# Optimization experiments

Hardware: AMD Instinct MI355X
Metric: run time of the kernel (lower is better)

Reference implementation:

```python
import jax, jax.numpy as jnp
import numpy as np

N_NODES = 100000
N_EDGES = 1600000
UNITS = 256
N_LAYERS = 4          # model_layers
NUM_GRAPHS = 512
IN_FEAT = 9


def _glorot(key, shape):
    lim = float(np.sqrt(6.0 / (shape[0] + shape[1])))
    return jax.random.uniform(key, shape, jnp.float32, -lim, lim)


def setup_inputs() -> dict:
    key = jax.random.key(0)
    ks = jax.random.split(key, 16)
    x = jax.random.normal(ks[0], (N_NODES, IN_FEAT), jnp.float32)
    edge_index = jax.random.randint(ks[1], (2, N_EDGES), 0, N_NODES, jnp.int64)
    batch = jnp.sort(jax.random.randint(ks[2], (N_NODES,), 0, NUM_GRAPHS, jnp.int64))
    Win = _glorot(ks[3], (IN_FEAT, UNITS))
    bin_ = jnp.zeros((UNITS,), jnp.float32)
    Ws = jnp.stack([_glorot(ks[4 + i], (UNITS, UNITS)) for i in range(N_LAYERS - 1)])
    bs = jnp.zeros((N_LAYERS - 1, UNITS), jnp.float32)
    fc1_w = _glorot(ks[8], (UNITS, UNITS))
    fc1_b = jnp.zeros((UNITS,), jnp.float32)
    fc2_w = _glorot(ks[9], (UNITS, 32))
    fc2_b = jnp.zeros((32,), jnp.float32)
    fc3_w = _glorot(ks[10], (32, 1))
    fc3_b = jnp.zeros((1,), jnp.float32)
    return dict(x=x, edge_index=edge_index, batch=batch, Win=Win, bin_=bin_,
                Ws=Ws, bs=bs, fc1_w=fc1_w, fc1_b=fc1_b, fc2_w=fc2_w,
                fc2_b=fc2_b, fc3_w=fc3_w, fc3_b=fc3_b)


def _gcn_conv(x, W, b, src, dst, dinv):
    # PyG GCNConv: h = xW ; out = D^-1/2 (A+I) D^-1/2 h + b  (self-loops added)
    h = x @ W                                     # [N, d]
    norm = dinv[src] * dinv[dst]                  # [E]
    agg = jnp.zeros_like(h).at[dst].add(h[src] * norm[:, None])
    agg = agg + h * (dinv * dinv)[:, None]        # self-loop term
    return agg + b


def reference(x, edge_index, batch, Win, bin_, Ws, bs,
              fc1_w, fc1_b, fc2_w, fc2_b, fc3_w, fc3_b):
    src, dst = edge_index[0], edge_index[1]
    # degree with self-loops
    deg = jnp.zeros((N_NODES,), jnp.float32).at[dst].add(1.0) + 1.0
    dinv = jax.lax.rsqrt(deg)

    h = jnp.tanh(_gcn_conv(x, Win, bin_, src, dst, dinv))
    for i in range(N_LAYERS - 1):
        h = jnp.tanh(_gcn_conv(h, Ws[i], bs[i], src, dst, dinv))
        # dropout: identity at inference
    h = jnp.tanh(h @ fc1_w + fc1_b)
    h = jnp.tanh(h @ fc2_w + fc2_b)
    h = h @ fc3_w + fc3_b                          # [N, 1]
    # global mean pool over graphs
    sums = jax.ops.segment_sum(h, batch, num_segments=NUM_GRAPHS)      # [G, 1]
    cnts = jax.ops.segment_sum(jnp.ones((N_NODES,), jnp.float32), batch,
                               num_segments=NUM_GRAPHS)
    pooled = sums / jnp.maximum(cnts, 1.0)[:, None]
    return jax.nn.sigmoid(pooled)
```

## Files before the change

kernel.cpp:

```cpp
#include <hip/hip_runtime.h>
#include <math.h>

#define N_NODES 100000
#define N_EDGES 1600000
#define UNITS   256
#define NGRAPH  512
#define IN_FEAT 9
#define NB_SCAN ((N_NODES + 255) / 256)
#define NBUK    ((N_NODES + 255) / 256)
#define BCAP    8192
#define EPB     16384
#define NPB     ((N_EDGES + EPB - 1) / EPB)

typedef short bf16x8 __attribute__((ext_vector_type(8)));
typedef float f32x4  __attribute__((ext_vector_type(4)));
typedef float f32x2  __attribute__((ext_vector_type(2)));

__device__ __forceinline__ float bflo(unsigned int u) {
  return __builtin_bit_cast(float, u << 16);
}
__device__ __forceinline__ float bfhi(unsigned int u) {
  return __builtin_bit_cast(float, u & 0xffff0000u);
}
__device__ __forceinline__ unsigned short f2bf(float f) {
  unsigned int u = __builtin_bit_cast(unsigned int, f);
  u += 0x7fffu + ((u >> 16) & 1u);
  return (unsigned short)(u >> 16);
}

__device__ __forceinline__ int swz(int row, int byteInRow) {
  return row * 128 + (byteInRow ^ ((row & 7) << 4));
}


__global__ __launch_bounds__(256) void k_part(const int* __restrict__ ei,
                                              int* __restrict__ bcnt,
                                              uint2* __restrict__ bstore) {
  __shared__ int hist[NBUK];
  __shared__ int base[NBUK];
  int tid = threadIdx.x;
  int e0 = blockIdx.x * EPB;
  for (int i = tid; i < NBUK; i += 256) hist[i] = 0;
  __syncthreads();
  #pragma unroll 4
  for (int j = 0; j < EPB / 256; ++j) {
    int e = e0 + j * 256 + tid;
    if (e < N_EDGES) atomicAdd(&hist[ei[N_EDGES + e] >> 8], 1);
  }
  __syncthreads();
  for (int i = tid; i < NBUK; i += 256) {
    int h = hist[i];
    base[i] = h ? atomicAdd(&bcnt[i], h) : 0;
    hist[i] = 0;
  }
  __syncthreads();
  #pragma unroll 4
  for (int j = 0; j < EPB / 256; ++j) {
    int e = e0 + j * 256 + tid;
    if (e < N_EDGES) {
      int s = ei[e];
      int d = ei[N_EDGES + e];
      int b = d >> 8;
      int pos = base[b] + atomicAdd(&hist[b], 1);
      bstore[(size_t)b * BCAP + pos] = make_uint2((unsigned)s, (unsigned)d);
    }
  }
}

__global__ __launch_bounds__(256) void k_cnt(const int* __restrict__ bcnt,
                                             const uint2* __restrict__ bstore,
                                             int* __restrict__ cnt) {
  __shared__ int h[256];
  int b = blockIdx.x, tid = threadIdx.x;
  h[tid] = 0;
  __syncthreads();
  int nE = bcnt[b];
  for (int i = tid; i < nE; i += 256)
    atomicAdd(&h[bstore[(size_t)b * BCAP + i].y & 255], 1);
  __syncthreads();
  int node = b * 256 + tid;
  if (node < N_NODES) cnt[node] = h[tid];
}

__global__ __launch_bounds__(256) void k_colfill(const int* __restrict__ bcnt,
                                                 const uint2* __restrict__ bstore,
                                                 const int* __restrict__ row_ptr,
                                                 int* __restrict__ col) {
  __shared__ int cur[256];
  int b = blockIdx.x, tid = threadIdx.x;
  int node = b * 256 + tid;
  cur[tid] = (node < N_NODES) ? row_ptr[node] : 0;
  __syncthreads();
  int nE = bcnt[b];
  for (int i = tid; i < nE; i += 256) {
    uint2 sd = bstore[(size_t)b * BCAP + i];
    int pos = atomicAdd(&cur[sd.y & 255], 1);
    col[pos] = (int)sd.x;
  }
}

__global__ __launch_bounds__(256) void k_bsum(const int* __restrict__ cnt,
                                              int* __restrict__ bsum) {
  __shared__ int wsS[4];
  int b = blockIdx.x, tid = threadIdx.x, lane = tid & 63, w = tid >> 6;
  int idx = b * 256 + tid;
  int s = (idx < N_NODES) ? cnt[idx] : 0;
  #pragma unroll
  for (int m = 32; m >= 1; m >>= 1) s += __shfl_xor(s, m);
  if (lane == 0) wsS[w] = s;
  __syncthreads();
  if (tid == 0) bsum[b] = wsS[0] + wsS[1] + wsS[2] + wsS[3];
}

__global__ __launch_bounds__(512) void k_bscan(int* __restrict__ bsum) {
  __shared__ int wsS[8];
  int tid = threadIdx.x, lane = tid & 63, w = tid >> 6;
  int v = (tid < NB_SCAN) ? bsum[tid] : 0;
  int s = v;
  #pragma unroll
  for (int off = 1; off < 64; off <<= 1) {
    int t = __shfl_up(s, off);
    if (lane >= off) s += t;
  }
  if (lane == 63) wsS[w] = s;
  __syncthreads();
  int woff = 0;
  #pragma unroll
  for (int i = 0; i < 8; ++i) woff += (i < w) ? wsS[i] : 0;
  if (tid < NB_SCAN) bsum[tid] = woff + s - v;
}

__global__ __launch_bounds__(256) void k_scan3(const int* __restrict__ cnt,
                                               const int* __restrict__ bsum,
                                               int* __restrict__ row_ptr) {
  __shared__ int wsS[4];
  int b = blockIdx.x, tid = threadIdx.x, lane = tid & 63, w = tid >> 6;
  int idx = b * 256 + tid;
  int v = (idx < N_NODES) ? cnt[idx] : 0;
  int s = v;
  #pragma unroll
  for (int off = 1; off < 64; off <<= 1) {
    int t = __shfl_up(s, off);
    if (lane >= off) s += t;
  }
  if (lane == 63) wsS[w] = s;
  __syncthreads();
  int woff = 0;
  #pragma unroll
  for (int i = 0; i < 4; ++i) woff += (i < w) ? wsS[i] : 0;
  if (idx < N_NODES) row_ptr[idx] = bsum[b] + woff + s - v;
  if (idx == 0) row_ptr[N_NODES] = N_EDGES;
}

__global__ void k_dinv(const int* __restrict__ cnt, float* __restrict__ dinv) {
  int n = blockIdx.x * blockDim.x + threadIdx.x;
  if (n < N_NODES) dinv[n] = rsqrtf((float)cnt[n] + 1.0f);
}

__global__ void k_bounds(const int* __restrict__ batch, int* __restrict__ starts) {
  int g = blockIdx.x * blockDim.x + threadIdx.x;
  if (g > NGRAPH) return;
  if (g == NGRAPH) { starts[g] = N_NODES; return; }
  int lo = 0, hi = N_NODES;
  while (lo < hi) { int m = (lo + hi) >> 1; if (batch[m] < g) lo = m + 1; else hi = m; }
  starts[g] = lo;
}


__global__ void k_cvtW(const float* __restrict__ Ws, const float* __restrict__ fc1_w,
                       unsigned short* __restrict__ Wt) {
  int idx = blockIdx.x * 256 + threadIdx.x;
  int m = idx >> 16;
  int r = idx & 65535;
  int n = r >> 8;
  int k = r & 255;
  const float* src = (m < 3) ? (Ws + (size_t)m * 65536) : fc1_w;
  Wt[idx] = f2bf(src[k * 256 + n]);
}

__global__ void k_cvtW2(const float* __restrict__ fc2_w, unsigned short* __restrict__ Wt2) {
  int idx = blockIdx.x * 256 + threadIdx.x;
  int n = idx >> 8;
  int k = idx & 255;
  Wt2[idx] = f2bf(fc2_w[k * 32 + n]);
}

__global__ void k_scalex(const float* __restrict__ x, const float* __restrict__ dinv,
                         float* __restrict__ xs) {
  int idx = blockIdx.x * blockDim.x + threadIdx.x;
  if (idx < N_NODES * IN_FEAT) xs[idx] = x[idx] * dinv[idx / IN_FEAT];
}


__global__ void k_agg9(const float* __restrict__ xs, const int* __restrict__ row_ptr,
                       const int* __restrict__ col, const float* __restrict__ dinv,
                       float* __restrict__ p0) {
  int n = blockIdx.x * blockDim.x + threadIdx.x;
  if (n >= N_NODES) return;
  float acc[IN_FEAT];
  #pragma unroll
  for (int j = 0; j < IN_FEAT; ++j) acc[j] = xs[n * IN_FEAT + j];
  int beg = row_ptr[n], end = row_ptr[n + 1];
  for (int e = beg; e < end; ++e) {
    int s = col[e];
    #pragma unroll
    for (int j = 0; j < IN_FEAT; ++j) acc[j] += xs[s * IN_FEAT + j];
  }
  float dn = dinv[n];
  #pragma unroll
  for (int j = 0; j < IN_FEAT; ++j) p0[n * IN_FEAT + j] = dn * acc[j];
}

__global__ __launch_bounds__(256) void k_agg256(
    const unsigned int* __restrict__ hs8,
    const int* __restrict__ row_ptr, const int* __restrict__ col,
    const float* __restrict__ dinv, unsigned short* __restrict__ p) {
  int wid = threadIdx.x >> 6;
  int lane = threadIdx.x & 63;
  int n = blockIdx.x * 4 + wid;
  if (n >= N_NODES) return;
  unsigned int q = hs8[(size_t)n * 64 + lane];
  f32x2 lo = __builtin_amdgcn_cvt_pk_f32_fp8(q, false);
  f32x2 hi = __builtin_amdgcn_cvt_pk_f32_fp8(q, true);
  float a0 = lo[0], a1 = lo[1], a2 = hi[0], a3 = hi[1];
  int e = row_ptr[n], end = row_ptr[n + 1];
  for (; e + 8 <= end; e += 8) {
    int s[8];
    unsigned int qq[8];
    #pragma unroll
    for (int j = 0; j < 8; ++j) s[j] = col[e + j];
    #pragma unroll
    for (int j = 0; j < 8; ++j) qq[j] = hs8[(size_t)s[j] * 64 + lane];
    #pragma unroll
    for (int j = 0; j < 8; ++j) {
      f32x2 l2 = __builtin_amdgcn_cvt_pk_f32_fp8(qq[j], false);
      f32x2 h2 = __builtin_amdgcn_cvt_pk_f32_fp8(qq[j], true);
      a0 += l2[0]; a1 += l2[1]; a2 += h2[0]; a3 += h2[1];
    }
  }
  if (e + 4 <= end) {
    int s[4];
    unsigned int qq[4];
    #pragma unroll
    for (int j = 0; j < 4; ++j) s[j] = col[e + j];
    #pragma unroll
    for (int j = 0; j < 4; ++j) qq[j] = hs8[(size_t)s[j] * 64 + lane];
    #pragma unroll
    for (int j = 0; j < 4; ++j) {
      f32x2 l2 = __builtin_amdgcn_cvt_pk_f32_fp8(qq[j], false);
      f32x2 h2 = __builtin_amdgcn_cvt_pk_f32_fp8(qq[j], true);
      a0 += l2[0]; a1 += l2[1]; a2 += h2[0]; a3 += h2[1];
    }
    e += 4;
  }
  for (; e < end; ++e) {
    unsigned int q0 = hs8[(size_t)col[e] * 64 + lane];
    f32x2 l2 = __builtin_amdgcn_cvt_pk_f32_fp8(q0, false);
    f32x2 h2 = __builtin_amdgcn_cvt_pk_f32_fp8(q0, true);
    a0 += l2[0]; a1 += l2[1]; a2 += h2[0]; a3 += h2[1];
  }
  float dn = dinv[n];
  uint2 o;
  o.x = (unsigned int)f2bf(dn * a0) | ((unsigned int)f2bf(dn * a1) << 16);
  o.y = (unsigned int)f2bf(dn * a2) | ((unsigned int)f2bf(dn * a3) << 16);
  *(uint2*)(p + (size_t)n * UNITS + lane * 4) = o;
}


__global__ __launch_bounds__(256) void k_gemm9(const float* __restrict__ p0,
                                               const float* __restrict__ Win,
                                               const float* __restrict__ bin,
                                               const float* __restrict__ scale,
                                               unsigned char* __restrict__ h8) {
  __shared__ float pS[32][IN_FEAT];
  int tid = threadIdx.x;
  int row0 = blockIdx.x * 32;
  for (int i = tid; i < 32 * IN_FEAT; i += 256) {
    int r = i / IN_FEAT;
    pS[r][i % IN_FEAT] = (row0 + r < N_NODES) ? p0[(size_t)row0 * IN_FEAT + i] : 0.0f;
  }
  float wcol[IN_FEAT];
  #pragma unroll
  for (int k = 0; k < IN_FEAT; ++k) wcol[k] = Win[k * UNITS + tid];
  float b = bin[tid];
  __syncthreads();
  for (int r = 0; r < 32; ++r) {
    int gr = row0 + r;
    if (gr >= N_NODES) break;
    float a = b;
    #pragma unroll
    for (int k = 0; k < IN_FEAT; ++k) a += pS[r][k] * wcol[k];
    float v = scale[gr] * tanhf(a);
    float vn = __shfl_xor(v, 1);
    if ((tid & 1) == 0) {
      unsigned int pk = __builtin_amdgcn_cvt_pk_fp8_f32(v, vn, 0, false);
      *(unsigned short*)(h8 + (size_t)gr * UNITS + tid) = (unsigned short)pk;
    }
  }
}

__global__ __launch_bounds__(256, 4) void k_gemm_bf16(
    const unsigned short* __restrict__ A,
    const unsigned short* __restrict__ Wt,
    const float* __restrict__ bias,
    const float* __restrict__ scale,
    void* __restrict__ Cout, int out_fp8,
    int M) {
  __shared__ __align__(16) char lds[33792];
  char* Bs = lds;
  unsigned short (*Cs)[264] = (unsigned short(*)[264])lds;

  const int tid = threadIdx.x;
  const int w = tid >> 6;
  const int l = tid & 63;
  const int l15 = l & 15;
  const int blk = l >> 4;
  const int wr = w >> 1, wc = w & 1;
  const int row0 = blockIdx.x * 64;

  const int sr = tid >> 3;
  const int sc = (tid & 7) * 16;

  const unsigned short* aRow[2];
  #pragma unroll
  for (int rf = 0; rf < 2; ++rf) {
    int gr = row0 + 32 * wr + rf * 16 + l15;
    if (gr >= M) gr = M - 1;
    aRow[rf] = A + (size_t)gr * UNITS + 8 * blk;
  }

  f32x4 acc[2][8];
  #pragma unroll
  for (int rf = 0; rf < 2; ++rf)
    #pragma unroll
    for (int cf = 0; cf < 8; ++cf) acc[rf][cf] = (f32x4){0.f, 0.f, 0.f, 0.f};

  for (int ks = 0; ks < 4; ++ks) {
    const int k0 = ks * 64;
    if (ks) __syncthreads();
    #pragma unroll
    for (int i = 0; i < 8; ++i) {
      int n = sr + i * 32;
      uint4 v = *(const uint4*)(Wt + (size_t)n * UNITS + k0 + (sc >> 1));
      *(uint4*)(Bs + swz(n, sc)) = v;
    }
    __syncthreads();
    #pragma unroll
    for (int kc = 0; kc < 2; ++kc) {
      bf16x8 a[2];
      #pragma unroll
      for (int rf = 0; rf < 2; ++rf)
        a[rf] = *(const bf16x8*)(aRow[rf] + k0 + kc * 32);
      #pragma unroll
      for (int cf = 0; cf < 8; ++cf) {
        bf16x8 b = *(const bf16x8*)(Bs + swz(128 * wc + cf * 16 + l15, kc * 64 + blk * 16));
        acc[0][cf] = __builtin_amdgcn_mfma_f32_16x16x32_bf16(a[0], b, acc[0][cf], 0, 0, 0);
        acc[1][cf] = __builtin_amdgcn_mfma_f32_16x16x32_bf16(a[1], b, acc[1][cf], 0, 0, 0);
      }
    }
  }

  __syncthreads();
  float dvv[2][4];
  #pragma unroll
  for (int rf = 0; rf < 2; ++rf)
    #pragma unroll
    for (int reg = 0; reg < 4; ++reg) {
      int gr = row0 + 32 * wr + rf * 16 + 4 * blk + reg;
      dvv[rf][reg] = scale ? scale[gr < M ? gr : M - 1] : 1.0f;
    }
  #pragma unroll
  for (int cf = 0; cf < 8; ++cf) {
    float bcol = bias[128 * wc + cf * 16 + l15];
    #pragma unroll
    for (int rf = 0; rf < 2; ++rf) {
      #pragma unroll
      for (int reg = 0; reg < 4; ++reg) {
        float v = dvv[rf][reg] * tanhf(acc[rf][cf][reg] + bcol);
        Cs[32 * wr + rf * 16 + 4 * blk + reg][128 * wc + cf * 16 + l15] = f2bf(v);
      }
    }
  }
  __syncthreads();
  if (out_fp8) {
    unsigned char* C8 = (unsigned char*)Cout;
    #pragma unroll
    for (int j = 0; j < 8; ++j) {
      int flat = tid + j * 256;
      int r = flat >> 5;
      int c = flat & 31;
      int gr = row0 + r;
      if (gr < M) {
        uint4 v = *(const uint4*)&Cs[r][c * 8];
        uint2 u;
        u.x = __builtin_amdgcn_cvt_pk_fp8_f32(bflo(v.x), bfhi(v.x), 0, false);
        u.x = __builtin_amdgcn_cvt_pk_fp8_f32(bflo(v.y), bfhi(v.y), u.x, true);
        u.y = __builtin_amdgcn_cvt_pk_fp8_f32(bflo(v.z), bfhi(v.z), 0, false);
        u.y = __builtin_amdgcn_cvt_pk_fp8_f32(bflo(v.w), bfhi(v.w), u.y, true);
        *(uint2*)(C8 + (size_t)gr * UNITS + c * 8) = u;
      }
    }
  } else {
    unsigned short* C = (unsigned short*)Cout;
    #pragma unroll
    for (int j = 0; j < 8; ++j) {
      int flat = tid + j * 256;
      int r = flat >> 5;
      int c = flat & 31;
      int gr = row0 + r;
      if (gr < M) {
        uint4 v = *(const uint4*)&Cs[r][c * 8];
        *(uint4*)(C + (size_t)gr * UNITS + c * 8) = v;
      }
    }
  }
}


__global__ __launch_bounds__(256) void k_fc23(
    const unsigned short* __restrict__ H,
    const unsigned short* __restrict__ Wt2,
    const float* __restrict__ b2,
    const float* __restrict__ w3, const float* __restrict__ b3,
    float* __restrict__ ns, int M) {
  const int tid = threadIdx.x;
  const int w = tid >> 6;
  const int l = tid & 63;
  const int l15 = l & 15;
  const int blk = l >> 4;
  const int row0 = blockIdx.x * 64 + 16 * w;

  int r = row0 + l15;
  int rc = r < M ? r : M - 1;
  const unsigned short* aPtr = H + (size_t)rc * UNITS + 8 * blk;
  const unsigned short* bPtr = Wt2 + (size_t)l15 * UNITS + 8 * blk;

  f32x4 acc0 = (f32x4){0.f, 0.f, 0.f, 0.f};
  f32x4 acc1 = (f32x4){0.f, 0.f, 0.f, 0.f};
  #pragma unroll
  for (int k0 = 0; k0 < UNITS; k0 += 32) {
    bf16x8 a  = *(const bf16x8*)(aPtr + k0);
    bf16x8 b0 = *(const bf16x8*)(bPtr + k0);
    bf16x8 b1 = *(const bf16x8*)(bPtr + 16 * UNITS + k0);
    acc0 = __builtin_amdgcn_mfma_f32_16x16x32_bf16(a, b0, acc0, 0, 0, 0);
    acc1 = __builtin_amdgcn_mfma_f32_16x16x32_bf16(a, b1, acc1, 0, 0, 0);
  }

  float c0 = b2[l15], c1 = b2[16 + l15];
  float w30 = w3[l15], w31 = w3[16 + l15];
  float b3v = b3[0];
  #pragma unroll
  for (int reg = 0; reg < 4; ++reg) {
    float part = tanhf(acc0[reg] + c0) * w30 + tanhf(acc1[reg] + c1) * w31;
    #pragma unroll
    for (int m = 8; m >= 1; m >>= 1) part += __shfl_xor(part, m);
    int gr = row0 + 4 * blk + reg;
    if (l15 == 0 && gr < M) ns[gr] = part + b3v;
  }
}

__global__ __launch_bounds__(64) void k_pool(const float* __restrict__ ns,
                                             const int* __restrict__ starts,
                                             float* __restrict__ out) {
  int g = blockIdx.x;
  int lane = threadIdx.x;
  int s = starts[g], e = starts[g + 1];
  float acc = 0.0f;
  for (int i = s + lane; i < e; i += 64) acc += ns[i];
  #pragma unroll
  for (int m = 32; m >= 1; m >>= 1) acc += __shfl_xor(acc, m);
  if (lane == 0) {
    float mean = acc / fmaxf((float)(e - s), 1.0f);
    out[g] = 1.0f / (1.0f + expf(-mean));
  }
}


extern "C" void kernel_launch(void* const* d_in, const int* in_sizes, int n_in,
                              void* d_out, int out_size, void* d_ws, size_t ws_size,
                              hipStream_t stream) {
  const float* x     = (const float*)d_in[0];
  const int*   ei    = (const int*)d_in[1];
  const int*   batch = (const int*)d_in[2];
  const float* Win   = (const float*)d_in[3];
  const float* bin_  = (const float*)d_in[4];
  const float* Ws    = (const float*)d_in[5];
  const float* bs    = (const float*)d_in[6];
  const float* fc1_w = (const float*)d_in[7];
  const float* fc1_b = (const float*)d_in[8];
  const float* fc2_w = (const float*)d_in[9];
  const float* fc2_b = (const float*)d_in[10];
  const float* fc3_w = (const float*)d_in[11];
  const float* fc3_b = (const float*)d_in[12];
  float* out = (float*)d_out;

  char* ws = (char*)d_ws;
  size_t off = 0;
  auto alloc = [&](size_t bytes) {
    size_t o = off;
    off = (off + bytes + 255) & ~(size_t)255;
    return o;
  };
  int*   cnt     = (int*)(ws + alloc(N_NODES * 4));
  int*   row_ptr = (int*)(ws + alloc((N_NODES + 1) * 4));
  float* dinv    = (float*)(ws + alloc(N_NODES * 4));
  int*   col     = (int*)(ws + alloc((size_t)N_EDGES * 4));
  int*   bsum    = (int*)(ws + alloc(NB_SCAN * 4));
  int*   bcnt    = (int*)(ws + alloc(NBUK * 4));
  uint2* bstore  = (uint2*)(ws + alloc((size_t)NBUK * BCAP * 8));
  int*   starts  = (int*)(ws + alloc((NGRAPH + 1) * 4));
  float* ns      = (float*)(ws + alloc(N_NODES * 4));
  float* xs      = (float*)(ws + alloc((size_t)N_NODES * IN_FEAT * 4));
  float* p0      = (float*)(ws + alloc((size_t)N_NODES * IN_FEAT * 4));
  unsigned short* Wt   = (unsigned short*)(ws + alloc((size_t)4 * UNITS * UNITS * 2));
  unsigned short* Wt2  = (unsigned short*)(ws + alloc((size_t)32 * UNITS * 2));
  unsigned char*  h8a  = (unsigned char*)(ws + alloc((size_t)N_NODES * UNITS));
  unsigned char*  h8b  = (unsigned char*)(ws + alloc((size_t)N_NODES * UNITS));
  unsigned short* pbf  = (unsigned short*)(ws + alloc((size_t)N_NODES * UNITS * 2));
  unsigned short* hbf  = (unsigned short*)(ws + alloc((size_t)N_NODES * UNITS * 2));

  hipMemsetAsync(bcnt, 0, NBUK * 4, stream);

  k_cvtW<<<(4 * UNITS * UNITS) / 256, 256, 0, stream>>>(Ws, fc1_w, Wt);
  k_cvtW2<<<32, 256, 0, stream>>>(fc2_w, Wt2);

  k_part<<<NPB, 256, 0, stream>>>(ei, bcnt, bstore);
  k_cnt<<<NBUK, 256, 0, stream>>>(bcnt, bstore, cnt);
  k_bsum<<<NB_SCAN, 256, 0, stream>>>(cnt, bsum);
  k_bscan<<<1, 512, 0, stream>>>(bsum);
  k_scan3<<<NB_SCAN, 256, 0, stream>>>(cnt, bsum, row_ptr);
  k_dinv<<<(N_NODES + 255) / 256, 256, 0, stream>>>(cnt, dinv);
  k_colfill<<<NBUK, 256, 0, stream>>>(bcnt, bstore, row_ptr, col);
  k_bounds<<<3, 256, 0, stream>>>(batch, starts);

  k_scalex<<<(N_NODES * IN_FEAT + 255) / 256, 256, 0, stream>>>(x, dinv, xs);
  k_agg9<<<(N_NODES + 255) / 256, 256, 0, stream>>>(xs, row_ptr, col, dinv, p0);
  k_gemm9<<<(N_NODES + 31) / 32, 256, 0, stream>>>(p0, Win, bin_, dinv, h8a);

  int ggrid = (N_NODES + 63) / 64;
  k_agg256<<<(N_NODES + 3) / 4, 256, 0, stream>>>((const unsigned int*)h8a, row_ptr, col, dinv, pbf);
  k_gemm_bf16<<<ggrid, 256, 0, stream>>>(pbf, Wt + (size_t)0 * UNITS * UNITS,
                                         bs + (size_t)0 * UNITS, dinv, h8b, 1, N_NODES);
  k_agg256<<<(N_NODES + 3) / 4, 256, 0, stream>>>((const unsigned int*)h8b, row_ptr, col, dinv, pbf);
  k_gemm_bf16<<<ggrid, 256, 0, stream>>>(pbf, Wt + (size_t)1 * UNITS * UNITS,
                                         bs + (size_t)1 * UNITS, dinv, h8a, 1, N_NODES);
  k_agg256<<<(N_NODES + 3) / 4, 256, 0, stream>>>((const unsigned int*)h8a, row_ptr, col, dinv, pbf);
  k_gemm_bf16<<<ggrid, 256, 0, stream>>>(pbf, Wt + (size_t)2 * UNITS * UNITS,
                                         bs + (size_t)2 * UNITS, nullptr, hbf, 0, N_NODES);

  k_gemm_bf16<<<ggrid, 256, 0, stream>>>(hbf, Wt + (size_t)3 * UNITS * UNITS,
                                         fc1_b, nullptr, pbf, 0, N_NODES);

  k_fc23<<<(N_NODES + 63) / 64, 256, 0, stream>>>(pbf, Wt2, fc2_b, fc3_w, fc3_b, ns, N_NODES);

  k_pool<<<NGRAPH, 64, 0, stream>>>(ns, starts, out);
}
```

Measured before the change: 561.9 us.

## Fuse neighbor aggregation into GEMM kernel via LDS-staged A tile

Merges the per-layer sparse aggregation kernel with the following dense bf16 GEMM. Each block gathers 64 node rows into a swizzled LDS A tile and multiplies it directly with the weights, so the bf16 aggregated buffer is never written to or read back from global memory. The cost is 64KB of LDS per block with a 2-blocks occupancy bound, and the gather phase can no longer overlap with other blocks' MFMA work as freely. The plain GEMM kernel is reduced to the fc1 case.

Result: slower. 888.6 us (+58.1%).

```diff
diff --git a/kernel.cpp b/kernel.cpp
--- a/kernel.cpp
+++ b/kernel.cpp
@@ -31,6 +31,9 @@
 __device__ __forceinline__ int swz(int row, int byteInRow) {
   return row * 128 + (byteInRow ^ ((row & 7) << 4));
 }
+__device__ __forceinline__ int swzA(int row, int byteInRow) {
+  return row * 512 + (byteInRow ^ ((row & 7) << 4));
+}
 
 
 __global__ __launch_bounds__(256) void k_part(const int* __restrict__ ei,
@@ -210,62 +213,6 @@
   #pragma unroll
   for (int j = 0; j < IN_FEAT; ++j) p0[n * IN_FEAT + j] = dn * acc[j];
 }
-
-__global__ __launch_bounds__(256) void k_agg256(
-    const unsigned int* __restrict__ hs8,
-    const int* __restrict__ row_ptr, const int* __restrict__ col,
-    const float* __restrict__ dinv, unsigned short* __restrict__ p) {
-  int wid = threadIdx.x >> 6;
-  int lane = threadIdx.x & 63;
-  int n = blockIdx.x * 4 + wid;
-  if (n >= N_NODES) return;
-  unsigned int q = hs8[(size_t)n * 64 + lane];
-  f32x2 lo = __builtin_amdgcn_cvt_pk_f32_fp8(q, false);
-  f32x2 hi = __builtin_amdgcn_cvt_pk_f32_fp8(q, true);
-  float a0 = lo[0], a1 = lo[1], a2 = hi[0], a3 = hi[1];
-  int e = row_ptr[n], end = row_ptr[n + 1];
-  for (; e + 8 <= end; e += 8) {
-    int s[8];
-    unsigned int qq[8];
-    #pragma unroll
-    for (int j = 0; j < 8; ++j) s[j] = col[e + j];
-    #pragma unroll
-    for (int j = 0; j < 8; ++j) qq[j] = hs8[(size_t)s[j] * 64 + lane];
-    #pragma unroll
-    for (int j = 0; j < 8; ++j) {
-      f32x2 l2 = __builtin_amdgcn_cvt_pk_f32_fp8(qq[j], false);
-      f32x2 h2 = __builtin_amdgcn_cvt_pk_f32_fp8(qq[j], true);
-      a0 += l2[0]; a1 += l2[1]; a2 += h2[0]; a3 += h2[1];
-    }
-  }
-  if (e + 4 <= end) {
-    int s[4];
-    unsigned int qq[4];
-    #pragma unroll
-    for (int j = 0; j < 4; ++j) s[j] = col[e + j];
-    #pragma unroll
-    for (int j = 0; j < 4; ++j) qq[j] = hs8[(size_t)s[j] * 64 + lane];
-    #pragma unroll
-    for (int j = 0; j < 4; ++j) {
-      f32x2 l2 = __builtin_amdgcn_cvt_pk_f32_fp8(qq[j], false);
-      f32x2 h2 = __builtin_amdgcn_cvt_pk_f32_fp8(qq[j], true);
-      a0 += l2[0]; a1 += l2[1]; a2 += h2[0]; a3 += h2[1];
-    }
-    e += 4;
-  }
-  for (; e < end; ++e) {
-    unsigned int q0 = hs8[(size_t)col[e] * 64 + lane];
-    f32x2 l2 = __builtin_amdgcn_cvt_pk_f32_fp8(q0, false);
-    f32x2 h2 = __builtin_amdgcn_cvt_pk_f32_fp8(q0, true);
-    a0 += l2[0]; a1 += l2[1]; a2 += h2[0]; a3 += h2[1];
-  }
-  float dn = dinv[n];
-  uint2 o;
-  o.x = (unsigned int)f2bf(dn * a0) | ((unsigned int)f2bf(dn * a1) << 16);
-  o.y = (unsigned int)f2bf(dn * a2) | ((unsigned int)f2bf(dn * a3) << 16);
-  *(uint2*)(p + (size_t)n * UNITS + lane * 4) = o;
-}
-
 
 __global__ __launch_bounds__(256) void k_gemm9(const float* __restrict__ p0,
                                                const float* __restrict__ Win,
@@ -299,12 +246,182 @@
   }
 }
 
+
+__global__ __launch_bounds__(256, 2) void k_agg_gemm(
+    const unsigned int* __restrict__ hs8,
+    const int* __restrict__ row_ptr, const int* __restrict__ col,
+    const float* __restrict__ dinv,
+    const unsigned short* __restrict__ Wt,
+    const float* __restrict__ bias,
+    const float* __restrict__ scale,
+    void* __restrict__ Cout, int out_fp8, int M) {
+  __shared__ __align__(16) char lds[65536];
+  char* As = lds;
+  char* Bs = lds + 32768;
+  unsigned short* CsA = (unsigned short*)lds;
+
+  const int tid = threadIdx.x;
+  const int w = tid >> 6;
+  const int lane = tid & 63;
+  const int l15 = lane & 15;
+  const int blk = lane >> 4;
+  const int wr = w >> 1, wc = w & 1;
+  const int row0 = blockIdx.x * 64;
+
+  for (int rr = 0; rr < 16; ++rr) {
+    int r = w * 16 + rr;
+    int n = row0 + r;
+    float a0 = 0.f, a1 = 0.f, a2 = 0.f, a3 = 0.f;
+    if (n < M) {
+      unsigned int q = hs8[(size_t)n * 64 + lane];
+      f32x2 lo = __builtin_amdgcn_cvt_pk_f32_fp8(q, false);
+      f32x2 hi = __builtin_amdgcn_cvt_pk_f32_fp8(q, true);
+      a0 = lo[0]; a1 = lo[1]; a2 = hi[0]; a3 = hi[1];
+      int e = row_ptr[n], end = row_ptr[n + 1];
+      for (; e + 8 <= end; e += 8) {
+        int s[8];
+        unsigned int qq[8];
+        #pragma unroll
+        for (int j = 0; j < 8; ++j) s[j] = col[e + j];
+        #pragma unroll
+        for (int j = 0; j < 8; ++j) qq[j] = hs8[(size_t)s[j] * 64 + lane];
+        #pragma unroll
+        for (int j = 0; j < 8; ++j) {
+          f32x2 l2 = __builtin_amdgcn_cvt_pk_f32_fp8(qq[j], false);
+          f32x2 h2 = __builtin_amdgcn_cvt_pk_f32_fp8(qq[j], true);
+          a0 += l2[0]; a1 += l2[1]; a2 += h2[0]; a3 += h2[1];
+        }
+      }
+      if (e + 4 <= end) {
+        int s[4];
+        unsigned int qq[4];
+        #pragma unroll
+        for (int j = 0; j < 4; ++j) s[j] = col[e + j];
+        #pragma unroll
+        for (int j = 0; j < 4; ++j) qq[j] = hs8[(size_t)s[j] * 64 + lane];
+        #pragma unroll
+        for (int j = 0; j < 4; ++j) {
+          f32x2 l2 = __builtin_amdgcn_cvt_pk_f32_fp8(qq[j], false);
+          f32x2 h2 = __builtin_amdgcn_cvt_pk_f32_fp8(qq[j], true);
+          a0 += l2[0]; a1 += l2[1]; a2 += h2[0]; a3 += h2[1];
+        }
+        e += 4;
+      }
+      for (; e < end; ++e) {
+        unsigned int q0 = hs8[(size_t)col[e] * 64 + lane];
+        f32x2 l2 = __builtin_amdgcn_cvt_pk_f32_fp8(q0, false);
+        f32x2 h2 = __builtin_amdgcn_cvt_pk_f32_fp8(q0, true);
+        a0 += l2[0]; a1 += l2[1]; a2 += h2[0]; a3 += h2[1];
+      }
+      float dn = dinv[n];
+      a0 *= dn; a1 *= dn; a2 *= dn; a3 *= dn;
+    }
+    uint2 o;
+    o.x = (unsigned int)f2bf(a0) | ((unsigned int)f2bf(a1) << 16);
+    o.y = (unsigned int)f2bf(a2) | ((unsigned int)f2bf(a3) << 16);
+    *(uint2*)(As + swzA(r, lane * 8)) = o;
+  }
+
+  const int sr = tid >> 3;
+  const int sc = (tid & 7) * 16;
+
+  f32x4 acc[2][8];
+  #pragma unroll
+  for (int rf = 0; rf < 2; ++rf)
+    #pragma unroll
+    for (int cf = 0; cf < 8; ++cf) acc[rf][cf] = (f32x4){0.f, 0.f, 0.f, 0.f};
+
+  for (int ks = 0; ks < 4; ++ks) {
+    const int k0 = ks * 64;
+    if (ks) __syncthreads();
+    #pragma unroll
+    for (int i = 0; i < 8; ++i) {
+      int n = sr + i * 32;
+      uint4 v = *(const uint4*)(Wt + (size_t)n * UNITS + k0 + (sc >> 1));
+      *(uint4*)(Bs + swz(n, sc)) = v;
+    }
+    __syncthreads();
+    #pragma unroll
+    for (int kc = 0; kc < 2; ++kc) {
+      bf16x8 a[2];
+      #pragma unroll
+      for (int rf = 0; rf < 2; ++rf) {
+        int ar = 32 * wr + rf * 16 + l15;
+        a[rf] = *(const bf16x8*)(As + swzA(ar, blk * 16 + ks * 128 + kc * 64));
+      }
+      #pragma unroll
+      for (int cf = 0; cf < 8; ++cf) {
+        bf16x8 b = *(const bf16x8*)(Bs + swz(128 * wc + cf * 16 + l15, kc * 64 + blk * 16));
+        acc[0][cf] = __builtin_amdgcn_mfma_f32_16x16x32_bf16(a[0], b, acc[0][cf], 0, 0, 0);
+        acc[1][cf] = __builtin_amdgcn_mfma_f32_16x16x32_bf16(a[1], b, acc[1][cf], 0, 0, 0);
+      }
+    }
+  }
+
+  __syncthreads();
+  float dvv[2][4];
+  #pragma unroll
+  for (int rf = 0; rf < 2; ++rf)
+    #pragma unroll
+    for (int reg = 0; reg < 4; ++reg) {
+      int gr = row0 + 32 * wr + rf * 16 + 4 * blk + reg;
+      dvv[rf][reg] = scale ? scale[gr < M ? gr : M - 1] : 1.0f;
+    }
+  #pragma unroll
+  for (int cf = 0; cf < 8; ++cf) {
+    float bcol = bias[128 * wc + cf * 16 + l15];
+    #pragma unroll
+    for (int rf = 0; rf < 2; ++rf) {
+      #pragma unroll
+      for (int reg = 0; reg < 4; ++reg) {
+        float v = dvv[rf][reg] * tanhf(acc[rf][cf][reg] + bcol);
+        int row = 32 * wr + rf * 16 + 4 * blk + reg;
+        int colb = (128 * wc + cf * 16 + l15) * 2;
+        *(unsigned short*)((char*)CsA + swzA(row, colb)) = f2bf(v);
+      }
+    }
+  }
+  __syncthreads();
+  if (out_fp8) {
+    unsigned char* C8 = (unsigned char*)Cout;
+    #pragma unroll
+    for (int j = 0; j < 8; ++j) {
+      int flat = tid + j * 256;
+      int r = flat >> 5;
+      int c = flat & 31;
+      int gr = row0 + r;
+      if (gr < M) {
+        uint4 v = *(const uint4*)((char*)CsA + swzA(r, c * 16));
+        uint2 u;
+        u.x = __builtin_amdgcn_cvt_pk_fp8_f32(bflo(v.x), bfhi(v.x), 0, false);
+        u.x = __builtin_amdgcn_cvt_pk_fp8_f32(bflo(v.y), bfhi(v.y), u.x, true);
+        u.y = __builtin_amdgcn_cvt_pk_fp8_f32(bflo(v.z), bfhi(v.z), 0, false);
+        u.y = __builtin_amdgcn_cvt_pk_fp8_f32(bflo(v.w), bfhi(v.w), u.y, true);
+        *(uint2*)(C8 + (size_t)gr * UNITS + c * 8) = u;
+      }
+    }
+  } else {
+    unsigned short* C = (unsigned short*)Cout;
+    #pragma unroll
+    for (int j = 0; j < 8; ++j) {
+      int flat = tid + j * 256;
+      int r = flat >> 5;
+      int c = flat & 31;
+      int gr = row0 + r;
+      if (gr < M) {
+        uint4 v = *(const uint4*)((char*)CsA + swzA(r, c * 16));
+        *(uint4*)(C + (size_t)gr * UNITS + c * 8) = v;
+      }
+    }
+  }
+}
+
+
 __global__ __launch_bounds__(256, 4) void k_gemm_bf16(
     const unsigned short* __restrict__ A,
     const unsigned short* __restrict__ Wt,
     const float* __restrict__ bias,
-    const float* __restrict__ scale,
-    void* __restrict__ Cout, int out_fp8,
+    unsigned short* __restrict__ C,
     int M) {
   __shared__ __align__(16) char lds[33792];
   char* Bs = lds;
@@ -361,14 +478,6 @@
   }
 
   __syncthreads();
-  float dvv[2][4];
-  #pragma unroll
-  for (int rf = 0; rf < 2; ++rf)
-    #pragma unroll
-    for (int reg = 0; reg < 4; ++reg) {
-      int gr = row0 + 32 * wr + rf * 16 + 4 * blk + reg;
-      dvv[rf][reg] = scale ? scale[gr < M ? gr : M - 1] : 1.0f;
-    }
   #pragma unroll
   for (int cf = 0; cf < 8; ++cf) {
     float bcol = bias[128 * wc + cf * 16 + l15];
@@ -376,42 +485,21 @@
     for (int rf = 0; rf < 2; ++rf) {
       #pragma unroll
       for (int reg = 0; reg < 4; ++reg) {
-        float v = dvv[rf][reg] * tanhf(acc[rf][cf][reg] + bcol);
+        float v = tanhf(acc[rf][cf][reg] + bcol);
         Cs[32 * wr + rf * 16 + 4 * blk + reg][128 * wc + cf * 16 + l15] = f2bf(v);
       }
     }
   }
   __syncthreads();
-  if (out_fp8) {
-    unsigned char* C8 = (unsigned char*)Cout;
-    #pragma unroll
-    for (int j = 0; j < 8; ++j) {
-      int flat = tid + j * 256;
-      int r = flat >> 5;
-      int c = flat & 31;
-      int gr = row0 + r;
-      if (gr < M) {
-        uint4 v = *(const uint4*)&Cs[r][c * 8];
-        uint2 u;
-        u.x = __builtin_amdgcn_cvt_pk_fp8_f32(bflo(v.x), bfhi(v.x), 0, false);
-        u.x = __builtin_amdgcn_cvt_pk_fp8_f32(bflo(v.y), bfhi(v.y), u.x, true);
-        u.y = __builtin_amdgcn_cvt_pk_fp8_f32(bflo(v.z), bfhi(v.z), 0, false);
-        u.y = __builtin_amdgcn_cvt_pk_fp8_f32(bflo(v.w), bfhi(v.w), u.y, true);
-        *(uint2*)(C8 + (size_t)gr * UNITS + c * 8) = u;
-      }
-    }
-  } else {
-    unsigned short* C = (unsigned short*)Cout;
-    #pragma unroll
-    for (int j = 0; j < 8; ++j) {
-      int flat = tid + j * 256;
-      int r = flat >> 5;
-      int c = flat & 31;
-      int gr = row0 + r;
-      if (gr < M) {
-        uint4 v = *(const uint4*)&Cs[r][c * 8];
-        *(uint4*)(C + (size_t)gr * UNITS + c * 8) = v;
-      }
+  #pragma unroll
+  for (int j = 0; j < 8; ++j) {
+    int flat = tid + j * 256;
+    int r = flat >> 5;
+    int c = flat & 31;
+    int gr = row0 + r;
+    if (gr < M) {
+      uint4 v = *(const uint4*)&Cs[r][c * 8];
+      *(uint4*)(C + (size_t)gr * UNITS + c * 8) = v;
     }
   }
 }
@@ -538,18 +626,18 @@
   k_gemm9<<<(N_NODES + 31) / 32, 256, 0, stream>>>(p0, Win, bin_, dinv, h8a);
 
   int ggrid = (N_NODES + 63) / 64;
-  k_agg256<<<(N_NODES + 3) / 4, 256, 0, stream>>>((const unsigned int*)h8a, row_ptr, col, dinv, pbf);
-  k_gemm_bf16<<<ggrid, 256, 0, stream>>>(pbf, Wt + (size_t)0 * UNITS * UNITS,
-                                         bs + (size_t)0 * UNITS, dinv, h8b, 1, N_NODES);
-  k_agg256<<<(N_NODES + 3) / 4, 256, 0, stream>>>((const unsigned int*)h8b, row_ptr, col, dinv, pbf);
-  k_gemm_bf16<<<ggrid, 256, 0, stream>>>(pbf, Wt + (size_t)1 * UNITS * UNITS,
-                                         bs + (size_t)1 * UNITS, dinv, h8a, 1, N_NODES);
-  k_agg256<<<(N_NODES + 3) / 4, 256, 0, stream>>>((const unsigned int*)h8a, row_ptr, col, dinv, pbf);
-  k_gemm_bf16<<<ggrid, 256, 0, stream>>>(pbf, Wt + (size_t)2 * UNITS * UNITS,
-                                         bs + (size_t)2 * UNITS, nullptr, hbf, 0, N_NODES);
+  k_agg_gemm<<<ggrid, 256, 0, stream>>>((const unsigned int*)h8a, row_ptr, col, dinv,
+                                        Wt + (size_t)0 * UNITS * UNITS,
+                                        bs + (size_t)0 * UNITS, dinv, h8b, 1, N_NODES);
+  k_agg_gemm<<<ggrid, 256, 0, stream>>>((const unsigned int*)h8b, row_ptr, col, dinv,
+                                        Wt + (size_t)1 * UNITS * UNITS,
+                                        bs + (size_t)1 * UNITS, dinv, h8a, 1, N_NODES);
+  k_agg_gemm<<<ggrid, 256, 0, stream>>>((const unsigned int*)h8a, row_ptr, col, dinv,
+                                        Wt + (size_t)2 * UNITS * UNITS,
+                                        bs + (size_t)2 * UNITS, nullptr, hbf, 0, N_NODES);
 
   k_gemm_bf16<<<ggrid, 256, 0, stream>>>(hbf, Wt + (size_t)3 * UNITS * UNITS,
-                                         fc1_b, nullptr, pbf, 0, N_NODES);
+                                         fc1_b, pbf, N_NODES);
 
   k_fc23<<<(N_NODES + 63) / 64, 256, 0, stream>>>(pbf, Wt2, fc2_b, fc3_w, fc3_b, ns, N_NODES);
 
```
